# Kernel optimization log

Hardware: AMD Instinct MI355X
Metric: run time of the kernel (lower is better)

## Reference

```python
import jax, jax.numpy as jnp
import numpy as np

N, E, IN_CH, OUT_CH, H, TOKEN_DIM, OPTION_NUM, N_GRAPHS = 50000, 800000, 128, 128, 4, 768, 4, 256
C = OUT_CH // H  # d_k = 32


def setup_inputs() -> dict:
    key = jax.random.key(0)
    ks = jax.random.split(key, 14)
    s = 0.02
    return {
        "x": jax.random.normal(ks[0], (N, IN_CH), jnp.float32),
        "edge_index": jax.random.randint(ks[1], (2, E), 0, N, jnp.int64),
        "sentence_embeddings": jax.random.normal(ks[2], (N_GRAPHS // OPTION_NUM, TOKEN_DIM), jnp.float32),
        "batch": jax.random.randint(ks[3], (N,), 0, N_GRAPHS, jnp.int64),
        "Wq": jax.random.normal(ks[4], (IN_CH, OUT_CH), jnp.float32) * s,
        "bq": jnp.zeros((OUT_CH,), jnp.float32),
        "Wk": jax.random.normal(ks[5], (IN_CH, OUT_CH), jnp.float32) * s,
        "bk": jnp.zeros((OUT_CH,), jnp.float32),
        "Wv": jax.random.normal(ks[6], (IN_CH, OUT_CH), jnp.float32) * s,
        "bv": jnp.zeros((OUT_CH,), jnp.float32),
        "Ws": jax.random.normal(ks[7], (TOKEN_DIM, OUT_CH), jnp.float32) * s,
        "bs": jnp.zeros((OUT_CH,), jnp.float32),
        "Wo": jax.random.normal(ks[8], (OUT_CH, OUT_CH), jnp.float32) * s,
        "bo": jnp.zeros((OUT_CH,), jnp.float32),
    }


def reference(x, edge_index, sentence_embeddings, batch, Wq, bq, Wk, bk, Wv, bv, Ws, bs, Wo, bo):
    sqdk = jnp.sqrt(jnp.asarray(C, jnp.float32))
    group = batch // OPTION_NUM                        # [N]
    Q = (x @ Wq + bq).reshape(-1, H, C)                # [N,H,C]
    K = (x @ Wk + bk).reshape(-1, H, C)
    V = (x @ Wv + bv).reshape(-1, H, C)
    sent = sentence_embeddings[group]                  # [N, token_dim]
    S = (sent @ Ws + bs).reshape(-1, H, C)             # Q_sentence == K_sentence (same linear)
    row, col = edge_index[0], edge_index[1]
    Qi, Kj, Vj = Q[row], K[col], V[col]                # [E,H,C] gathers
    Si, Sj = S[row], S[col]
    # (qk + qs_k + q_ks)/sqdk averaged over 3 terms
    alpha = ((Qi * Kj).sum(-1) + (Si * Kj).sum(-1) + (Qi * Sj).sum(-1)) / (sqdk * 3.0)  # [E,H]
    alpha = jax.nn.leaky_relu(alpha, negative_slope=0.2)
    alpha = jax.nn.softmax(alpha, axis=0)              # global softmax over all edges per head (as original)
    out = jnp.zeros_like(V).at[row].add(Vj * alpha[..., None])  # scatter-add to target nodes
    out = out.reshape(-1, H * C) @ Wo + bo
    return out + x  # in_channels == out_channels -> residual_lin is None
```

## Files before the change

kernel.cpp:

```cpp
#include <hip/hip_runtime.h>
#include <hip/hip_fp16.h>
#include <hip/hip_bf16.h>


typedef __attribute__((ext_vector_type(8))) short bfx8;
typedef __attribute__((ext_vector_type(4))) float f32x4;

__device__ __forceinline__ unsigned short f2bf(float f) {
    union { float f; unsigned int u; } v; v.f = f;
    unsigned int r = v.u + 0x7fffu + ((v.u >> 16) & 1u);
    return (unsigned short)(r >> 16);
}
__device__ __forceinline__ float bf2f(unsigned short u) {
    union { unsigned int u; float f; } v; v.u = ((unsigned int)u) << 16;
    return v.f;
}

__device__ __forceinline__ float4 ld4(const float* p, int i) {
    return ((const float4*)p)[i];
}
__device__ __forceinline__ float4 ld4(const __half* p, int i) {
    __half2 h01 = ((const __half2*)p)[2 * i];
    __half2 h23 = ((const __half2*)p)[2 * i + 1];
    float2 a = __half22float2(h01);
    float2 b = __half22float2(h23);
    return make_float4(a.x, a.y, b.x, b.y);
}
__device__ __forceinline__ void st1(float* p, float v) { *p = v; }
__device__ __forceinline__ void st1(__half* p, float v) { *p = __float2half_rn(v); }

__global__ void k_sgemm(const float* __restrict__ sent, const float* __restrict__ Ws,
                        const float* __restrict__ bs, float* __restrict__ Sg) {
    int g = blockIdx.x;
    int o = threadIdx.x;
    const float* s = sent + g * 768;
    float acc = 0.f;
    #pragma unroll 8
    for (int k = 0; k < 768; ++k) acc += s[k] * Ws[k * 128 + o];
    Sg[g * 128 + o] = acc + bs[o];
}

__global__ __launch_bounds__(256) void k_wsplit(
    const float* __restrict__ Wq, const float* __restrict__ Wk,
    const float* __restrict__ Wv, const float* __restrict__ bq,
    const float* __restrict__ bk, const float* __restrict__ bv,
    unsigned short* __restrict__ wfrag, float* __restrict__ bcat) {
    int gid = blockIdx.x * 256 + threadIdx.x;
    if (gid < 384)
        bcat[gid] = (gid < 128) ? bq[gid] : (gid < 256) ? bk[gid - 128] : bv[gid - 256];
    int l = gid & 63;
    int fk = gid >> 6;
    int ks = fk & 3, ng = fk >> 2;
    int n = ng * 16 + (l & 15);
    const float* W = (n < 128) ? Wq : (n < 256) ? Wk : Wv;
    int col = n & 127;
    int kbase = ks * 32 + (l >> 4) * 8;
    bfx8 hv, lv;
    #pragma unroll
    for (int e = 0; e < 8; ++e) {
        float v = W[(size_t)(kbase + e) * 128 + col];
        unsigned short h = f2bf(v);
        hv[e] = (short)h;
        lv[e] = (short)f2bf(v - bf2f(h));
    }
    ((bfx8*)wfrag)[fk * 64 + l] = hv;
    ((bfx8*)wfrag)[6144 + fk * 64 + l] = lv;
}

__global__ __launch_bounds__(256) void k_qkv_mfma(
    const float* __restrict__ x, const int* __restrict__ batch,
    const unsigned short* __restrict__ wfrag, const float* __restrict__ bcat,
    float* __restrict__ pack, unsigned char* __restrict__ group8, int N) {
    __shared__ __align__(16) unsigned short hi_lds[32 * 128];
    __shared__ __align__(16) unsigned short lo_lds[32 * 128];

    const int tid = threadIdx.x;
    const int row0 = blockIdx.x * 32;

    const float4* x4 = (const float4*)x;
    #pragma unroll
    for (int t = tid; t < 512; t += 256) {
        int r = t >> 4, u = t & 15;
        int row = row0 + r;
        float4 a = make_float4(0.f, 0.f, 0.f, 0.f), b = a;
        if (row < N) {
            a = x4[(size_t)row * 32 + u * 2];
            b = x4[(size_t)row * 32 + u * 2 + 1];
        }
        float v[8] = {a.x, a.y, a.z, a.w, b.x, b.y, b.z, b.w};
        bfx8 hv, lv;
        #pragma unroll
        for (int e = 0; e < 8; ++e) {
            unsigned short h = f2bf(v[e]);
            hv[e] = (short)h;
            lv[e] = (short)f2bf(v[e] - bf2f(h));
        }
        int su = r * 16 + (u ^ (r & 7));
        ((bfx8*)hi_lds)[su] = hv;
        ((bfx8*)lo_lds)[su] = lv;
    }
    if (tid < 32) {
        int row = row0 + tid;
        if (row < N) group8[row] = (unsigned char)(batch[row] >> 2);
    }
    __syncthreads();

    const int w = tid >> 6;
    const int l = tid & 63;
    const int l15 = l & 15, lh = l >> 4;

    f32x4 zero = {0.f, 0.f, 0.f, 0.f};
    f32x4 acc[2][6];
    #pragma unroll
    for (int m = 0; m < 2; ++m)
        #pragma unroll
        for (int n = 0; n < 6; ++n) acc[m][n] = zero;

    const bfx8* wf = (const bfx8*)wfrag;
    const bfx8* hi8 = (const bfx8*)hi_lds;
    const bfx8* lo8 = (const bfx8*)lo_lds;

    #pragma unroll
    for (int ks = 0; ks < 4; ++ks) {
        bfx8 bh[6], bl[6];
        #pragma unroll
        for (int n = 0; n < 6; ++n) {
            int fk = (w * 6 + n) * 4 + ks;
            bh[n] = wf[fk * 64 + l];
            bl[n] = wf[6144 + fk * 64 + l];
        }
        bfx8 ah[2], al[2];
        #pragma unroll
        for (int m = 0; m < 2; ++m) {
            int r = m * 16 + l15;
            int su = r * 16 + ((ks * 4 + lh) ^ (r & 7));
            ah[m] = hi8[su];
            al[m] = lo8[su];
        }
        #pragma unroll
        for (int m = 0; m < 2; ++m)
            #pragma unroll
            for (int n = 0; n < 6; ++n) {
                acc[m][n] = __builtin_amdgcn_mfma_f32_16x16x32_bf16(ah[m], bh[n], acc[m][n], 0, 0, 0);
                acc[m][n] = __builtin_amdgcn_mfma_f32_16x16x32_bf16(ah[m], bl[n], acc[m][n], 0, 0, 0);
                acc[m][n] = __builtin_amdgcn_mfma_f32_16x16x32_bf16(al[m], bh[n], acc[m][n], 0, 0, 0);
            }
    }

    #pragma unroll
    for (int n = 0; n < 6; ++n) {
        int colg = w * 96 + n * 16 + l15;
        float bias = bcat[colg];
        #pragma unroll
        for (int m = 0; m < 2; ++m) {
            int rbase = row0 + m * 16 + lh * 4;
            #pragma unroll
            for (int j = 0; j < 4; ++j) {
                int rr = rbase + j;
                if (rr < N) pack[(size_t)rr * 384 + colg] = acc[m][n][j] + bias;
            }
        }
    }
}

template <typename T>
__global__ __launch_bounds__(256) void k_qkv(
    const float* __restrict__ x, const int* __restrict__ batch,
    const float* __restrict__ Wq, const float* __restrict__ bq,
    const float* __restrict__ Wk, const float* __restrict__ bk,
    const float* __restrict__ Wv, const float* __restrict__ bv,
    T* __restrict__ pack, unsigned char* __restrict__ group8, int N) {
    __shared__ float4 xs[32][32];

    const int row0 = blockIdx.x * 32;
    const int tid = threadIdx.x;

    for (int i = tid; i < 32 * 32; i += 256) {
        int r = i >> 5, k4 = i & 31;
        int row = row0 + r;
        float4 v = make_float4(0.f, 0.f, 0.f, 0.f);
        if (row < N) v = ((const float4*)x)[(size_t)row * 32 + k4];
        xs[r][k4] = v;
    }
    if (tid < 32) {
        int row = row0 + tid;
        if (row < N) group8[row] = (unsigned char)(batch[row] >> 2);
    }
    __syncthreads();

    const int o = tid & 127;
    const int half_ = tid >> 7;

    const float* Wm[3] = {Wq, Wk, Wv};
    const float* bm[3] = {bq, bk, bv};

    #pragma unroll
    for (int m = 0; m < 3; ++m) {
        const float* __restrict__ W = Wm[m];
        float acc[16];
        #pragma unroll
        for (int r = 0; r < 16; ++r) acc[r] = 0.f;
        for (int k4 = 0; k4 < 32; ++k4) {
            float w0 = W[(k4 * 4 + 0) * 128 + o];
            float w1 = W[(k4 * 4 + 1) * 128 + o];
            float w2 = W[(k4 * 4 + 2) * 128 + o];
            float w3 = W[(k4 * 4 + 3) * 128 + o];
            #pragma unroll
            for (int r = 0; r < 16; ++r) {
                float4 xv = xs[half_ * 16 + r][k4];
                acc[r] += xv.x * w0 + xv.y * w1 + xv.z * w2 + xv.w * w3;
            }
        }
        float b = bm[m][o];
        #pragma unroll
        for (int r = 0; r < 16; ++r) {
            int row = row0 + half_ * 16 + r;
            if (row >= N) continue;
            st1(&pack[(size_t)row * 384 + m * 128 + o], acc[r] + b);
        }
    }
}

__global__ __launch_bounds__(256) void k_hist(const int* __restrict__ eidx,
                                              int* __restrict__ counts, int E) {
    int e = blockIdx.x * 256 + threadIdx.x;
    if (e < E) atomicAdd(&counts[eidx[e]], 1);
}

__global__ __launch_bounds__(1024) void k_scan(const int* __restrict__ counts,
                                               int* __restrict__ row_start,
                                               int* __restrict__ cursor, int N) {
    __shared__ int part[1024];
    const int tid = threadIdx.x;
    const int chunk = (N + 1023) >> 10;
    const int lo = tid * chunk;
    const int hi = min(lo + chunk, N);
    int s = 0;
    for (int i = lo; i < hi; ++i) s += counts[i];
    part[tid] = s;
    __syncthreads();
    for (int d = 1; d < 1024; d <<= 1) {
        int v = 0;
        if (tid >= d) v = part[tid - d];
        __syncthreads();
        if (tid >= d) part[tid] += v;
        __syncthreads();
    }
    int run = (tid == 0) ? 0 : part[tid - 1];
    for (int i = lo; i < hi; ++i) {
        row_start[i] = run;
        cursor[i] = run;
        run += counts[i];
    }
    if (tid == 0) row_start[N] = part[1023];
}

__global__ __launch_bounds__(256) void k_scatter(const int* __restrict__ eidx,
                                                 int* __restrict__ cursor,
                                                 int* __restrict__ csr_col, int E) {
    int e = blockIdx.x * 256 + threadIdx.x;
    if (e < E) {
        int row = eidx[e];
        int col = eidx[E + e];
        int pos = atomicAdd(&cursor[row], 1);
        csr_col[pos] = col;
    }
}

template <typename T>
__global__ __launch_bounds__(512, 4) void k_rowedge(
    const int* __restrict__ csr_col, const int* __restrict__ row_start,
    const T* __restrict__ pack, const unsigned char* __restrict__ group8,
    const float* __restrict__ Sg, float* __restrict__ outacc,
    double* __restrict__ head_sum, int N) {
    __shared__ float4 sg4[64 * 32];
    __shared__ float hsum[4];

    const int tid = threadIdx.x;
    for (int i = tid; i < 64 * 32; i += 512) sg4[i] = ((const float4*)Sg)[i];
    if (tid < 4) hsum[tid] = 0.f;
    __syncthreads();

    const int wid = tid >> 6;
    const int l = tid & 63;
    const int half = l >> 5;
    const int hl = l & 31;
    const int row = blockIdx.x * 8 + wid;

    const float inv_scale = 0.05892556509887896f;
    float lsum = 0.f;

    if (row < N) {
        const T* rp = pack + (size_t)row * 384;
        float4 q = ld4(rp, hl);
        float4 sr = sg4[(int)group8[row] * 32 + hl];
        float4 qs = make_float4(q.x + sr.x, q.y + sr.y, q.z + sr.z, q.w + sr.w);
        float4 acc = make_float4(0.f, 0.f, 0.f, 0.f);

        const int beg = row_start[row];
        const int end = row_start[row + 1];
        for (int i = beg + half; i < end; i += 4) {
            const int iB = i + 2;
            const bool vB = iB < end;
            int colA = csr_col[i];
            int colB = vB ? csr_col[iB] : colA;
            const T* cpA = pack + (size_t)colA * 384;
            const T* cpB = pack + (size_t)colB * 384;
            float4 kkA = ld4(cpA + 128, hl);
            float4 vvA = ld4(cpA + 256, hl);
            float4 kkB = ld4(cpB + 128, hl);
            float4 vvB = ld4(cpB + 256, hl);
            float4 scA = sg4[(int)group8[colA] * 32 + hl];
            float4 scB = sg4[(int)group8[colB] * 32 + hl];

            float tA = qs.x * kkA.x + qs.y * kkA.y + qs.z * kkA.z + qs.w * kkA.w
                     + q.x * scA.x + q.y * scA.y + q.z * scA.z + q.w * scA.w;
            float tB = qs.x * kkB.x + qs.y * kkB.y + qs.z * kkB.z + qs.w * kkB.w
                     + q.x * scB.x + q.y * scB.y + q.z * scB.z + q.w * scB.w;
            tA += __shfl_xor(tA, 1);  tB += __shfl_xor(tB, 1);
            tA += __shfl_xor(tA, 2);  tB += __shfl_xor(tB, 2);
            tA += __shfl_xor(tA, 4);  tB += __shfl_xor(tB, 4);

            float aA = tA * inv_scale;
            aA = (aA >= 0.f) ? aA : 0.2f * aA;
            float aB = tB * inv_scale;
            aB = (aB >= 0.f) ? aB : 0.2f * aB;
            float pA = expf(aA);
            float pB = vB ? expf(aB) : 0.f;

            if ((hl & 7) == 0) lsum += pA + pB;
            acc.x += pA * vvA.x + pB * vvB.x;
            acc.y += pA * vvA.y + pB * vvB.y;
            acc.z += pA * vvA.z + pB * vvB.z;
            acc.w += pA * vvA.w + pB * vvB.w;
        }

        acc.x += __shfl_xor(acc.x, 32);
        acc.y += __shfl_xor(acc.y, 32);
        acc.z += __shfl_xor(acc.z, 32);
        acc.w += __shfl_xor(acc.w, 32);
        if (half == 0)
            ((float4*)(outacc + (size_t)row * 128))[hl] = acc;
    }

    if ((l & 7) == 0) atomicAdd(&hsum[(l & 31) >> 3], lsum);
    __syncthreads();
    if (tid < 4) atomicAdd(&head_sum[tid], (double)hsum[tid]);
}

__global__ __launch_bounds__(256) void k_out(
    const float* __restrict__ outacc, const double* __restrict__ head_sum,
    const float* __restrict__ Wo, const float* __restrict__ bo,
    const float* __restrict__ x, float* __restrict__ out, int N) {
    __shared__ float4 ys[32][32];

    const int row0 = blockIdx.x * 32;
    const int tid = threadIdx.x;

    float inv[4];
    #pragma unroll
    for (int hh = 0; hh < 4; ++hh) inv[hh] = (float)(1.0 / head_sum[hh]);

    for (int i = tid; i < 32 * 32; i += 256) {
        int r = i >> 5, k4 = i & 31;
        int row = row0 + r;
        float4 v = make_float4(0.f, 0.f, 0.f, 0.f);
        if (row < N) v = ((const float4*)outacc)[(size_t)row * 32 + k4];
        float s = inv[k4 >> 3];
        v.x *= s; v.y *= s; v.z *= s; v.w *= s;
        ys[r][k4] = v;
    }
    __syncthreads();

    const int o = tid & 127;
    const int half_ = tid >> 7;
    float acc[16];
    #pragma unroll
    for (int r = 0; r < 16; ++r) acc[r] = 0.f;
    for (int k4 = 0; k4 < 32; ++k4) {
        float w0 = Wo[(k4 * 4 + 0) * 128 + o];
        float w1 = Wo[(k4 * 4 + 1) * 128 + o];
        float w2 = Wo[(k4 * 4 + 2) * 128 + o];
        float w3 = Wo[(k4 * 4 + 3) * 128 + o];
        #pragma unroll
        for (int r = 0; r < 16; ++r) {
            float4 yv = ys[half_ * 16 + r][k4];
            acc[r] += yv.x * w0 + yv.y * w1 + yv.z * w2 + yv.w * w3;
        }
    }
    float b = bo[o];
    #pragma unroll
    for (int r = 0; r < 16; ++r) {
        int row = row0 + half_ * 16 + r;
        if (row < N)
            out[(size_t)row * 128 + o] = acc[r] + b + x[(size_t)row * 128 + o];
    }
}

extern "C" void kernel_launch(void* const* d_in, const int* in_sizes, int n_in,
                              void* d_out, int out_size, void* d_ws, size_t ws_size,
                              hipStream_t stream) {
    const float* x     = (const float*)d_in[0];
    const int*   eidx  = (const int*)d_in[1];
    const float* sent  = (const float*)d_in[2];
    const int*   batch = (const int*)d_in[3];
    const float* Wq = (const float*)d_in[4];
    const float* bq = (const float*)d_in[5];
    const float* Wk = (const float*)d_in[6];
    const float* bk = (const float*)d_in[7];
    const float* Wv = (const float*)d_in[8];
    const float* bv = (const float*)d_in[9];
    const float* Ws = (const float*)d_in[10];
    const float* bs = (const float*)d_in[11];
    const float* Wo = (const float*)d_in[12];
    const float* bo = (const float*)d_in[13];

    const int N = in_sizes[0] / 128;
    const int E = in_sizes[1] / 2;

    char* ws = (char*)d_ws;
    size_t off = 0;
    auto alloc = [&](size_t bytes) {
        char* p = ws + off;
        off += (bytes + 255) & ~(size_t)255;
        return p;
    };
    float*  Sg        = (float*)alloc(64 * 128 * sizeof(float));
    double* head_sum  = (double*)alloc(4 * sizeof(double));
    unsigned char* group8 = (unsigned char*)alloc((size_t)N);
    int* counts    = (int*)alloc((size_t)N * sizeof(int));
    int* row_start = (int*)alloc(((size_t)N + 1) * sizeof(int));
    int* cursor    = (int*)alloc((size_t)N * sizeof(int));
    int* csr_col   = (int*)alloc((size_t)E * sizeof(int));
    unsigned short* wfrag = (unsigned short*)alloc(2 * 96 * 64 * 8 * sizeof(unsigned short));
    float* bcat    = (float*)alloc(384 * sizeof(float));
    size_t pack_off = off;
    size_t need_f32 = pack_off + (size_t)N * 384 * sizeof(float);
    bool use_f32 = (ws_size >= need_f32);

    float* outacc = (float*)d_out;

    hipMemsetAsync(counts, 0, (size_t)N * sizeof(int), stream);
    hipMemsetAsync(head_sum, 0, 4 * sizeof(double), stream);

    k_sgemm<<<64, 128, 0, stream>>>(sent, Ws, bs, Sg);

    const int eb = (E + 255) / 256;
    k_hist<<<eb, 256, 0, stream>>>(eidx, counts, E);
    k_scan<<<1, 1024, 0, stream>>>(counts, row_start, cursor, N);
    k_scatter<<<eb, 256, 0, stream>>>(eidx, cursor, csr_col, E);

    const int qkv_blocks = (N + 31) / 32;
    const int row_blocks = (N + 7) / 8;
    if (use_f32) {
        float* pack = (float*)(ws + pack_off);
        k_wsplit<<<24, 256, 0, stream>>>(Wq, Wk, Wv, bq, bk, bv, wfrag, bcat);
        k_qkv_mfma<<<qkv_blocks, 256, 0, stream>>>(x, batch, wfrag, bcat,
                                                   pack, group8, N);
        k_rowedge<float><<<row_blocks, 512, 0, stream>>>(csr_col, row_start, pack,
                                                         group8, Sg, outacc,
                                                         head_sum, N);
    } else {
        __half* pack = (__half*)(ws + pack_off);
        k_qkv<__half><<<qkv_blocks, 256, 0, stream>>>(x, batch, Wq, bq, Wk, bk,
                                                      Wv, bv, pack, group8, N);
        k_rowedge<__half><<<row_blocks, 512, 0, stream>>>(csr_col, row_start, pack,
                                                          group8, Sg, outacc,
                                                          head_sum, N);
    }

    k_out<<<qkv_blocks, 256, 0, stream>>>(outacc, head_sum, Wo, bo, x,
                                          (float*)d_out, N);
}
```

Measured before the change: 534.5 us.

## Store QKV pack in fp16, fuse prep kernels, use MFMA for output projection

The QKV projection always writes an fp16 pack instead of fp32, which halves the bytes gathered per edge in the row-edge kernel. The sentence GEMM, the weight split into bf16 hi/lo fragments (now also covering Wo) and the edge histogram are merged into one prep launch. The output projection now uses the split-bf16 MFMA path instead of scalar FMA. The cost is fp16 rounding of Q/K/V, which may loosen accuracy against the fp32 reference.

```diff
diff --git a/kernel.cpp b/kernel.cpp
--- a/kernel.cpp
+++ b/kernel.cpp
@@ -15,216 +15,67 @@
     union { unsigned int u; float f; } v; v.u = ((unsigned int)u) << 16;
     return v.f;
 }
-
-__device__ __forceinline__ float4 ld4(const float* p, int i) {
-    return ((const float4*)p)[i];
-}
-__device__ __forceinline__ float4 ld4(const __half* p, int i) {
-    __half2 h01 = ((const __half2*)p)[2 * i];
-    __half2 h23 = ((const __half2*)p)[2 * i + 1];
-    float2 a = __half22float2(h01);
-    float2 b = __half22float2(h23);
+__device__ __forceinline__ float4 ld4h(const __half* p) {
+    float2 raw = *(const float2*)p;
+    union { float2 f; __half2 h[2]; } u; u.f = raw;
+    float2 a = __half22float2(u.h[0]);
+    float2 b = __half22float2(u.h[1]);
     return make_float4(a.x, a.y, b.x, b.y);
 }
-__device__ __forceinline__ void st1(float* p, float v) { *p = v; }
-__device__ __forceinline__ void st1(__half* p, float v) { *p = __float2half_rn(v); }
-
-__global__ void k_sgemm(const float* __restrict__ sent, const float* __restrict__ Ws,
-                        const float* __restrict__ bs, float* __restrict__ Sg) {
-    int g = blockIdx.x;
-    int o = threadIdx.x;
-    const float* s = sent + g * 768;
-    float acc = 0.f;
-    #pragma unroll 8
-    for (int k = 0; k < 768; ++k) acc += s[k] * Ws[k * 128 + o];
-    Sg[g * 128 + o] = acc + bs[o];
-}
-
-__global__ __launch_bounds__(256) void k_wsplit(
+
+__global__ __launch_bounds__(256) void k_prep(
+    const float* __restrict__ sent, const float* __restrict__ Ws,
+    const float* __restrict__ bs, float* __restrict__ Sg,
     const float* __restrict__ Wq, const float* __restrict__ Wk,
-    const float* __restrict__ Wv, const float* __restrict__ bq,
-    const float* __restrict__ bk, const float* __restrict__ bv,
-    unsigned short* __restrict__ wfrag, float* __restrict__ bcat) {
-    int gid = blockIdx.x * 256 + threadIdx.x;
-    if (gid < 384)
-        bcat[gid] = (gid < 128) ? bq[gid] : (gid < 256) ? bk[gid - 128] : bv[gid - 256];
-    int l = gid & 63;
-    int fk = gid >> 6;
-    int ks = fk & 3, ng = fk >> 2;
-    int n = ng * 16 + (l & 15);
-    const float* W = (n < 128) ? Wq : (n < 256) ? Wk : Wv;
-    int col = n & 127;
-    int kbase = ks * 32 + (l >> 4) * 8;
-    bfx8 hv, lv;
-    #pragma unroll
-    for (int e = 0; e < 8; ++e) {
-        float v = W[(size_t)(kbase + e) * 128 + col];
-        unsigned short h = f2bf(v);
-        hv[e] = (short)h;
-        lv[e] = (short)f2bf(v - bf2f(h));
-    }
-    ((bfx8*)wfrag)[fk * 64 + l] = hv;
-    ((bfx8*)wfrag)[6144 + fk * 64 + l] = lv;
-}
-
-__global__ __launch_bounds__(256) void k_qkv_mfma(
-    const float* __restrict__ x, const int* __restrict__ batch,
-    const unsigned short* __restrict__ wfrag, const float* __restrict__ bcat,
-    float* __restrict__ pack, unsigned char* __restrict__ group8, int N) {
-    __shared__ __align__(16) unsigned short hi_lds[32 * 128];
-    __shared__ __align__(16) unsigned short lo_lds[32 * 128];
-
+    const float* __restrict__ Wv, const float* __restrict__ Wo,
+    const float* __restrict__ bq, const float* __restrict__ bk,
+    const float* __restrict__ bv, const float* __restrict__ bo,
+    unsigned short* __restrict__ wfrag, float* __restrict__ bcat,
+    const int* __restrict__ eidx, int* __restrict__ counts, int E) {
+    const int b = blockIdx.x;
     const int tid = threadIdx.x;
-    const int row0 = blockIdx.x * 32;
-
-    const float4* x4 = (const float4*)x;
-    #pragma unroll
-    for (int t = tid; t < 512; t += 256) {
-        int r = t >> 4, u = t & 15;
-        int row = row0 + r;
-        float4 a = make_float4(0.f, 0.f, 0.f, 0.f), b = a;
-        if (row < N) {
-            a = x4[(size_t)row * 32 + u * 2];
-            b = x4[(size_t)row * 32 + u * 2 + 1];
-        }
-        float v[8] = {a.x, a.y, a.z, a.w, b.x, b.y, b.z, b.w};
+    if (b < 32) {
+        int g = b * 2 + (tid >> 7);
+        int o = tid & 127;
+        const float* s = sent + g * 768;
+        float acc = 0.f;
+        #pragma unroll 8
+        for (int k = 0; k < 768; ++k) acc += s[k] * Ws[k * 128 + o];
+        Sg[g * 128 + o] = acc + bs[o];
+    } else if (b < 64) {
+        int gid = (b - 32) * 256 + tid;
+        if (gid < 512)
+            bcat[gid] = (gid < 128) ? bq[gid]
+                      : (gid < 256) ? bk[gid - 128]
+                      : (gid < 384) ? bv[gid - 256] : bo[gid - 384];
+        int l = gid & 63;
+        int fk = gid >> 6;
+        int ks = fk & 3;
+        const float* W;
+        int col;
+        if (fk < 96) {
+            int n = (fk >> 2) * 16 + (l & 15);
+            W = (n < 128) ? Wq : (n < 256) ? Wk : Wv;
+            col = n & 127;
+        } else {
+            col = ((fk - 96) >> 2) * 16 + (l & 15);
+            W = Wo;
+        }
+        int kbase = ks * 32 + (l >> 4) * 8;
         bfx8 hv, lv;
         #pragma unroll
         for (int e = 0; e < 8; ++e) {
-            unsigned short h = f2bf(v[e]);
+            float v = W[(size_t)(kbase + e) * 128 + col];
+            unsigned short h = f2bf(v);
             hv[e] = (short)h;
-            lv[e] = (short)f2bf(v[e] - bf2f(h));
-        }
-        int su = r * 16 + (u ^ (r & 7));
-        ((bfx8*)hi_lds)[su] = hv;
-        ((bfx8*)lo_lds)[su] = lv;
-    }
-    if (tid < 32) {
-        int row = row0 + tid;
-        if (row < N) group8[row] = (unsigned char)(batch[row] >> 2);
-    }
-    __syncthreads();
-
-    const int w = tid >> 6;
-    const int l = tid & 63;
-    const int l15 = l & 15, lh = l >> 4;
-
-    f32x4 zero = {0.f, 0.f, 0.f, 0.f};
-    f32x4 acc[2][6];
-    #pragma unroll
-    for (int m = 0; m < 2; ++m)
-        #pragma unroll
-        for (int n = 0; n < 6; ++n) acc[m][n] = zero;
-
-    const bfx8* wf = (const bfx8*)wfrag;
-    const bfx8* hi8 = (const bfx8*)hi_lds;
-    const bfx8* lo8 = (const bfx8*)lo_lds;
-
-    #pragma unroll
-    for (int ks = 0; ks < 4; ++ks) {
-        bfx8 bh[6], bl[6];
-        #pragma unroll
-        for (int n = 0; n < 6; ++n) {
-            int fk = (w * 6 + n) * 4 + ks;
-            bh[n] = wf[fk * 64 + l];
-            bl[n] = wf[6144 + fk * 64 + l];
-        }
-        bfx8 ah[2], al[2];
-        #pragma unroll
-        for (int m = 0; m < 2; ++m) {
-            int r = m * 16 + l15;
-            int su = r * 16 + ((ks * 4 + lh) ^ (r & 7));
-            ah[m] = hi8[su];
-            al[m] = lo8[su];
-        }
-        #pragma unroll
-        for (int m = 0; m < 2; ++m)
-            #pragma unroll
-            for (int n = 0; n < 6; ++n) {
-                acc[m][n] = __builtin_amdgcn_mfma_f32_16x16x32_bf16(ah[m], bh[n], acc[m][n], 0, 0, 0);
-                acc[m][n] = __builtin_amdgcn_mfma_f32_16x16x32_bf16(ah[m], bl[n], acc[m][n], 0, 0, 0);
-                acc[m][n] = __builtin_amdgcn_mfma_f32_16x16x32_bf16(al[m], bh[n], acc[m][n], 0, 0, 0);
-            }
-    }
-
-    #pragma unroll
-    for (int n = 0; n < 6; ++n) {
-        int colg = w * 96 + n * 16 + l15;
-        float bias = bcat[colg];
-        #pragma unroll
-        for (int m = 0; m < 2; ++m) {
-            int rbase = row0 + m * 16 + lh * 4;
-            #pragma unroll
-            for (int j = 0; j < 4; ++j) {
-                int rr = rbase + j;
-                if (rr < N) pack[(size_t)rr * 384 + colg] = acc[m][n][j] + bias;
-            }
-        }
-    }
-}
-
-template <typename T>
-__global__ __launch_bounds__(256) void k_qkv(
-    const float* __restrict__ x, const int* __restrict__ batch,
-    const float* __restrict__ Wq, const float* __restrict__ bq,
-    const float* __restrict__ Wk, const float* __restrict__ bk,
-    const float* __restrict__ Wv, const float* __restrict__ bv,
-    T* __restrict__ pack, unsigned char* __restrict__ group8, int N) {
-    __shared__ float4 xs[32][32];
-
-    const int row0 = blockIdx.x * 32;
-    const int tid = threadIdx.x;
-
-    for (int i = tid; i < 32 * 32; i += 256) {
-        int r = i >> 5, k4 = i & 31;
-        int row = row0 + r;
-        float4 v = make_float4(0.f, 0.f, 0.f, 0.f);
-        if (row < N) v = ((const float4*)x)[(size_t)row * 32 + k4];
-        xs[r][k4] = v;
-    }
-    if (tid < 32) {
-        int row = row0 + tid;
-        if (row < N) group8[row] = (unsigned char)(batch[row] >> 2);
-    }
-    __syncthreads();
-
-    const int o = tid & 127;
-    const int half_ = tid >> 7;
-
-    const float* Wm[3] = {Wq, Wk, Wv};
-    const float* bm[3] = {bq, bk, bv};
-
-    #pragma unroll
-    for (int m = 0; m < 3; ++m) {
-        const float* __restrict__ W = Wm[m];
-        float acc[16];
-        #pragma unroll
-        for (int r = 0; r < 16; ++r) acc[r] = 0.f;
-        for (int k4 = 0; k4 < 32; ++k4) {
-            float w0 = W[(k4 * 4 + 0) * 128 + o];
-            float w1 = W[(k4 * 4 + 1) * 128 + o];
-            float w2 = W[(k4 * 4 + 2) * 128 + o];
-            float w3 = W[(k4 * 4 + 3) * 128 + o];
-            #pragma unroll
-            for (int r = 0; r < 16; ++r) {
-                float4 xv = xs[half_ * 16 + r][k4];
-                acc[r] += xv.x * w0 + xv.y * w1 + xv.z * w2 + xv.w * w3;
-            }
-        }
-        float b = bm[m][o];
-        #pragma unroll
-        for (int r = 0; r < 16; ++r) {
-            int row = row0 + half_ * 16 + r;
-            if (row >= N) continue;
-            st1(&pack[(size_t)row * 384 + m * 128 + o], acc[r] + b);
-        }
-    }
-}
-
-__global__ __launch_bounds__(256) void k_hist(const int* __restrict__ eidx,
-                                              int* __restrict__ counts, int E) {
-    int e = blockIdx.x * 256 + threadIdx.x;
-    if (e < E) atomicAdd(&counts[eidx[e]], 1);
+            lv[e] = (short)f2bf(v - bf2f(h));
+        }
+        ((bfx8*)wfrag)[fk * 64 + l] = hv;
+        ((bfx8*)wfrag)[8192 + fk * 64 + l] = lv;
+    } else {
+        int e = (b - 64) * 256 + tid;
+        if (e < E) atomicAdd(&counts[eidx[e]], 1);
+    }
 }
 
 __global__ __launch_bounds__(1024) void k_scan(const int* __restrict__ counts,
@@ -267,10 +118,106 @@
     }
 }
 
-template <typename T>
+__global__ __launch_bounds__(256) void k_qkv_mfma(
+    const float* __restrict__ x, const int* __restrict__ batch,
+    const unsigned short* __restrict__ wfrag, const float* __restrict__ bcat,
+    __half* __restrict__ pack, unsigned char* __restrict__ group8, int N) {
+    __shared__ __align__(16) unsigned short hi_lds[32 * 128];
+    __shared__ __align__(16) unsigned short lo_lds[32 * 128];
+
+    const int tid = threadIdx.x;
+    const int row0 = blockIdx.x * 32;
+
+    const float4* x4 = (const float4*)x;
+    #pragma unroll
+    for (int t = tid; t < 512; t += 256) {
+        int r = t >> 4, u = t & 15;
+        int row = row0 + r;
+        float4 a = make_float4(0.f, 0.f, 0.f, 0.f), b = a;
+        if (row < N) {
+            a = x4[(size_t)row * 32 + u * 2];
+            b = x4[(size_t)row * 32 + u * 2 + 1];
+        }
+        float v[8] = {a.x, a.y, a.z, a.w, b.x, b.y, b.z, b.w};
+        bfx8 hv, lv;
+        #pragma unroll
+        for (int e = 0; e < 8; ++e) {
+            unsigned short h = f2bf(v[e]);
+            hv[e] = (short)h;
+            lv[e] = (short)f2bf(v[e] - bf2f(h));
+        }
+        int su = r * 16 + (u ^ (r & 7));
+        ((bfx8*)hi_lds)[su] = hv;
+        ((bfx8*)lo_lds)[su] = lv;
+    }
+    if (tid < 32) {
+        int row = row0 + tid;
+        if (row < N) group8[row] = (unsigned char)(batch[row] >> 2);
+    }
+    __syncthreads();
+
+    const int w = tid >> 6;
+    const int l = tid & 63;
+    const int l15 = l & 15, lh = l >> 4;
+
+    f32x4 zero = {0.f, 0.f, 0.f, 0.f};
+    f32x4 acc[2][6];
+    #pragma unroll
+    for (int m = 0; m < 2; ++m)
+        #pragma unroll
+        for (int n = 0; n < 6; ++n) acc[m][n] = zero;
+
+    const bfx8* wf = (const bfx8*)wfrag;
+    const bfx8* hi8 = (const bfx8*)hi_lds;
+    const bfx8* lo8 = (const bfx8*)lo_lds;
+
+    #pragma unroll
+    for (int ks = 0; ks < 4; ++ks) {
+        bfx8 bh[6], bl[6];
+        #pragma unroll
+        for (int n = 0; n < 6; ++n) {
+            int fk = (w * 6 + n) * 4 + ks;
+            bh[n] = wf[fk * 64 + l];
+            bl[n] = wf[8192 + fk * 64 + l];
+        }
+        bfx8 ah[2], al[2];
+        #pragma unroll
+        for (int m = 0; m < 2; ++m) {
+            int r = m * 16 + l15;
+            int su = r * 16 + ((ks * 4 + lh) ^ (r & 7));
+            ah[m] = hi8[su];
+            al[m] = lo8[su];
+        }
+        #pragma unroll
+        for (int m = 0; m < 2; ++m)
+            #pragma unroll
+            for (int n = 0; n < 6; ++n) {
+                acc[m][n] = __builtin_amdgcn_mfma_f32_16x16x32_bf16(ah[m], bh[n], acc[m][n], 0, 0, 0);
+                acc[m][n] = __builtin_amdgcn_mfma_f32_16x16x32_bf16(ah[m], bl[n], acc[m][n], 0, 0, 0);
+                acc[m][n] = __builtin_amdgcn_mfma_f32_16x16x32_bf16(al[m], bh[n], acc[m][n], 0, 0, 0);
+            }
+    }
+
+    #pragma unroll
+    for (int n = 0; n < 6; ++n) {
+        int colg = w * 96 + n * 16 + l15;
+        float bias = bcat[colg];
+        #pragma unroll
+        for (int m = 0; m < 2; ++m) {
+            int rbase = row0 + m * 16 + lh * 4;
+            #pragma unroll
+            for (int j = 0; j < 4; ++j) {
+                int rr = rbase + j;
+                if (rr < N)
+                    pack[(size_t)rr * 384 + colg] = __float2half_rn(acc[m][n][j] + bias);
+            }
+        }
+    }
+}
+
 __global__ __launch_bounds__(512, 4) void k_rowedge(
     const int* __restrict__ csr_col, const int* __restrict__ row_start,
-    const T* __restrict__ pack, const unsigned char* __restrict__ group8,
+    const __half* __restrict__ pack, const unsigned char* __restrict__ group8,
     const float* __restrict__ Sg, float* __restrict__ outacc,
     double* __restrict__ head_sum, int N) {
     __shared__ float4 sg4[64 * 32];
@@ -291,8 +238,8 @@
     float lsum = 0.f;
 
     if (row < N) {
-        const T* rp = pack + (size_t)row * 384;
-        float4 q = ld4(rp, hl);
+        const __half* rp = pack + (size_t)row * 384;
+        float4 q = ld4h(rp + 4 * hl);
         float4 sr = sg4[(int)group8[row] * 32 + hl];
         float4 qs = make_float4(q.x + sr.x, q.y + sr.y, q.z + sr.z, q.w + sr.w);
         float4 acc = make_float4(0.f, 0.f, 0.f, 0.f);
@@ -304,12 +251,12 @@
             const bool vB = iB < end;
             int colA = csr_col[i];
             int colB = vB ? csr_col[iB] : colA;
-            const T* cpA = pack + (size_t)colA * 384;
-            const T* cpB = pack + (size_t)colB * 384;
-            float4 kkA = ld4(cpA + 128, hl);
-            float4 vvA = ld4(cpA + 256, hl);
-            float4 kkB = ld4(cpB + 128, hl);
-            float4 vvB = ld4(cpB + 256, hl);
+            const __half* cpA = pack + (size_t)colA * 384;
+            const __half* cpB = pack + (size_t)colB * 384;
+            float4 kkA = ld4h(cpA + 128 + 4 * hl);
+            float4 vvA = ld4h(cpA + 256 + 4 * hl);
+            float4 kkB = ld4h(cpB + 128 + 4 * hl);
+            float4 vvB = ld4h(cpB + 256 + 4 * hl);
             float4 scA = sg4[(int)group8[colA] * 32 + hl];
             float4 scB = sg4[(int)group8[colB] * 32 + hl];
 
@@ -348,52 +295,103 @@
     if (tid < 4) atomicAdd(&head_sum[tid], (double)hsum[tid]);
 }
 
-__global__ __launch_bounds__(256) void k_out(
+__global__ __launch_bounds__(256) void k_out_mfma(
     const float* __restrict__ outacc, const double* __restrict__ head_sum,
-    const float* __restrict__ Wo, const float* __restrict__ bo,
+    const unsigned short* __restrict__ wfrag, const float* __restrict__ bcat,
     const float* __restrict__ x, float* __restrict__ out, int N) {
-    __shared__ float4 ys[32][32];
-
+    __shared__ __align__(16) unsigned short hi_lds[32 * 128];
+    __shared__ __align__(16) unsigned short lo_lds[32 * 128];
+
+    const int tid = threadIdx.x;
     const int row0 = blockIdx.x * 32;
-    const int tid = threadIdx.x;
 
     float inv[4];
     #pragma unroll
-    for (int hh = 0; hh < 4; ++hh) inv[hh] = (float)(1.0 / head_sum[hh]);
-
-    for (int i = tid; i < 32 * 32; i += 256) {
-        int r = i >> 5, k4 = i & 31;
+    for (int h = 0; h < 4; ++h) inv[h] = (float)(1.0 / head_sum[h]);
+
+    const float4* o4 = (const float4*)outacc;
+    #pragma unroll
+    for (int t = tid; t < 512; t += 256) {
+        int r = t >> 4, u = t & 15;
         int row = row0 + r;
-        float4 v = make_float4(0.f, 0.f, 0.f, 0.f);
-        if (row < N) v = ((const float4*)outacc)[(size_t)row * 32 + k4];
-        float s = inv[k4 >> 3];
-        v.x *= s; v.y *= s; v.z *= s; v.w *= s;
-        ys[r][k4] = v;
+        float4 a = make_float4(0.f, 0.f, 0.f, 0.f), b = a;
+        if (row < N) {
+            a = o4[(size_t)row * 32 + u * 2];
+            b = o4[(size_t)row * 32 + u * 2 + 1];
+        }
+        float s = inv[u >> 2];
+        float v[8] = {a.x * s, a.y * s, a.z * s, a.w * s,
+                      b.x * s, b.y * s, b.z * s, b.w * s};
+        bfx8 hv, lv;
+        #pragma unroll
+        for (int e = 0; e < 8; ++e) {
+            unsigned short h = f2bf(v[e]);
+            hv[e] = (short)h;
+            lv[e] = (short)f2bf(v[e] - bf2f(h));
+        }
+        int su = r * 16 + (u ^ (r & 7));
+        ((bfx8*)hi_lds)[su] = hv;
+        ((bfx8*)lo_lds)[su] = lv;
     }
     __syncthreads();
 
-    const int o = tid & 127;
-    const int half_ = tid >> 7;
-    float acc[16];
-    #pragma unroll
-    for (int r = 0; r < 16; ++r) acc[r] = 0.f;
-    for (int k4 = 0; k4 < 32; ++k4) {
-        float w0 = Wo[(k4 * 4 + 0) * 128 + o];
-        float w1 = Wo[(k4 * 4 + 1) * 128 + o];
-        float w2 = Wo[(k4 * 4 + 2) * 128 + o];
-        float w3 = Wo[(k4 * 4 + 3) * 128 + o];
-        #pragma unroll
-        for (int r = 0; r < 16; ++r) {
-            float4 yv = ys[half_ * 16 + r][k4];
-            acc[r] += yv.x * w0 + yv.y * w1 + yv.z * w2 + yv.w * w3;
-        }
-    }
-    float b = bo[o];
-    #pragma unroll
-    for (int r = 0; r < 16; ++r) {
-        int row = row0 + half_ * 16 + r;
-        if (row < N)
-            out[(size_t)row * 128 + o] = acc[r] + b + x[(size_t)row * 128 + o];
+    const int w = tid >> 6;
+    const int l = tid & 63;
+    const int l15 = l & 15, lh = l >> 4;
+
+    f32x4 zero = {0.f, 0.f, 0.f, 0.f};
+    f32x4 acc[2][2];
+    #pragma unroll
+    for (int m = 0; m < 2; ++m)
+        #pragma unroll
+        for (int n = 0; n < 2; ++n) acc[m][n] = zero;
+
+    const bfx8* wf = (const bfx8*)wfrag;
+    const bfx8* hi8 = (const bfx8*)hi_lds;
+    const bfx8* lo8 = (const bfx8*)lo_lds;
+
+    #pragma unroll
+    for (int ks = 0; ks < 4; ++ks) {
+        bfx8 bh[2], bl[2];
+        #pragma unroll
+        for (int n = 0; n < 2; ++n) {
+            int fk = 96 + (w * 2 + n) * 4 + ks;
+            bh[n] = wf[fk * 64 + l];
+            bl[n] = wf[8192 + fk * 64 + l];
+        }
+        bfx8 ah[2], al[2];
+        #pragma unroll
+        for (int m = 0; m < 2; ++m) {
+            int r = m * 16 + l15;
+            int su = r * 16 + ((ks * 4 + lh) ^ (r & 7));
+            ah[m] = hi8[su];
+            al[m] = lo8[su];
+        }
+        #pragma unroll
+        for (int m = 0; m < 2; ++m)
+            #pragma unroll
+            for (int n = 0; n < 2; ++n) {
+                acc[m][n] = __builtin_amdgcn_mfma_f32_16x16x32_bf16(ah[m], bh[n], acc[m][n], 0, 0, 0);
+                acc[m][n] = __builtin_amdgcn_mfma_f32_16x16x32_bf16(ah[m], bl[n], acc[m][n], 0, 0, 0);
+                acc[m][n] = __builtin_amdgcn_mfma_f32_16x16x32_bf16(al[m], bh[n], acc[m][n], 0, 0, 0);
+            }
+    }
+
+    #pragma unroll
+    for (int n = 0; n < 2; ++n) {
+        int colg = w * 32 + n * 16 + l15;
+        float bias = bcat[384 + colg];
+        #pragma unroll
+        for (int m = 0; m < 2; ++m) {
+            int rbase = row0 + m * 16 + lh * 4;
+            #pragma unroll
+            for (int j = 0; j < 4; ++j) {
+                int rr = rbase + j;
+                if (rr < N)
+                    out[(size_t)rr * 128 + colg] =
+                        acc[m][n][j] + bias + x[(size_t)rr * 128 + colg];
+            }
+        }
     }
 }
 
@@ -432,43 +430,28 @@
     int* row_start = (int*)alloc(((size_t)N + 1) * sizeof(int));
     int* cursor    = (int*)alloc((size_t)N * sizeof(int));
     int* csr_col   = (int*)alloc((size_t)E * sizeof(int));
-    unsigned short* wfrag = (unsigned short*)alloc(2 * 96 * 64 * 8 * sizeof(unsigned short));
-    float* bcat    = (float*)alloc(384 * sizeof(float));
-    size_t pack_off = off;
-    size_t need_f32 = pack_off + (size_t)N * 384 * sizeof(float);
-    bool use_f32 = (ws_size >= need_f32);
+    unsigned short* wfrag = (unsigned short*)alloc(2 * 128 * 64 * 8 * sizeof(unsigned short));
+    float* bcat    = (float*)alloc(512 * sizeof(float));
+    __half* pack   = (__half*)alloc((size_t)N * 384 * sizeof(__half));
 
     float* outacc = (float*)d_out;
 
     hipMemsetAsync(counts, 0, (size_t)N * sizeof(int), stream);
     hipMemsetAsync(head_sum, 0, 4 * sizeof(double), stream);
 
-    k_sgemm<<<64, 128, 0, stream>>>(sent, Ws, bs, Sg);
-
     const int eb = (E + 255) / 256;
-    k_hist<<<eb, 256, 0, stream>>>(eidx, counts, E);
+    k_prep<<<64 + eb, 256, 0, stream>>>(sent, Ws, bs, Sg, Wq, Wk, Wv, Wo,
+                                        bq, bk, bv, bo, wfrag, bcat,
+                                        eidx, counts, E);
     k_scan<<<1, 1024, 0, stream>>>(counts, row_start, cursor, N);
     k_scatter<<<eb, 256, 0, stream>>>(eidx, cursor, csr_col, E);
 
     const int qkv_blocks = (N + 31) / 32;
     const int row_blocks = (N + 7) / 8;
-    if (use_f32) {
-        float* pack = (float*)(ws + pack_off);
-        k_wsplit<<<24, 256, 0, stream>>>(Wq, Wk, Wv, bq, bk, bv, wfrag, bcat);
-        k_qkv_mfma<<<qkv_blocks, 256, 0, stream>>>(x, batch, wfrag, bcat,
-                                                   pack, group8, N);
-        k_rowedge<float><<<row_blocks, 512, 0, stream>>>(csr_col, row_start, pack,
-                                                         group8, Sg, outacc,
-                                                         head_sum, N);
-    } else {
-        __half* pack = (__half*)(ws + pack_off);
-        k_qkv<__half><<<qkv_blocks, 256, 0, stream>>>(x, batch, Wq, bq, Wk, bk,
-                                                      Wv, bv, pack, group8, N);
-        k_rowedge<__half><<<row_blocks, 512, 0, stream>>>(csr_col, row_start, pack,
-                                                          group8, Sg, outacc,
-                                                          head_sum, N);
-    }
-
-    k_out<<<qkv_blocks, 256, 0, stream>>>(outacc, head_sum, Wo, bo, x,
-                                          (float*)d_out, N);
-}
+    k_qkv_mfma<<<qkv_blocks, 256, 0, stream>>>(x, batch, wfrag, bcat,
+                                               pack, group8, N);
+    k_rowedge<<<row_blocks, 512, 0, stream>>>(csr_col, row_start, pack,
+                                              group8, Sg, outacc, head_sum, N);
+    k_out_mfma<<<qkv_blocks, 256, 0, stream>>>(outacc, head_sum, wfrag, bcat,
+                                               x, (float*)d_out, N);
+}
```

New measurement: 467.7 us. 1.14x faster.
